# Kernel optimization log

Hardware: AMD Instinct MI355X
Metric: run time of the kernel (lower is better)

Reference implementation:

```python
import jax, jax.numpy as jnp
import numpy as np

N_NODES = 1000000


def setup_inputs() -> dict:
    key = jax.random.key(0)
    k1, k2, k3 = jax.random.split(key, 3)
    x = jax.random.normal(k1, (N_NODES, 16), dtype=jnp.float32)
    edge_index = jax.random.randint(k2, (2, 4000000), 0, N_NODES, dtype=jnp.int64)
    W = jax.random.normal(k3, (16, 16), dtype=jnp.float32) * (1.0 / np.sqrt(16.0))
    b = jnp.zeros((16,), dtype=jnp.float32)
    return {"x": x, "edge_index": edge_index, "W": W, "b": b}


def reference(x, edge_index, W, b):
    # GCNConv forward: out = D^{-1/2} (A + I) D^{-1/2} (x @ W) + b
    n = x.shape[0]
    row, col = edge_index[0], edge_index[1]  # src, dst

    h = x @ W  # [N, out]

    # degree on target nodes, including self-loops
    deg = jax.ops.segment_sum(jnp.ones_like(col, dtype=h.dtype), col, num_segments=n) + 1.0
    dinv = jax.lax.rsqrt(deg)  # deg >= 1 thanks to self-loops

    # per-edge symmetric normalization, gather-scale-scatter
    norm = dinv[row] * dinv[col]  # [E]
    msgs = h[row] * norm[:, None]  # [E, out]
    agg = jax.ops.segment_sum(msgs, col, num_segments=n)

    # self-loop contribution: norm_ii = dinv[i]^2
    out = agg + h * (dinv * dinv)[:, None] + b
    return out
```

## Files before the change

### kernel.cpp

```cpp
#include <hip/hip_runtime.h>


#define F 16
#define TILE 2048
#define TSHIFT 11
#define NBMAX 512
#define CAP 9728
#define EPT 19
#define CHUNK 8192
#define CUR_STRIDE 16

static __device__ __forceinline__ unsigned short f2bf(float f) {
    unsigned u = __float_as_uint(f);
    unsigned r = (u + 0x7FFFu + ((u >> 16) & 1u)) >> 16;
    return (unsigned short)r;
}
static __device__ __forceinline__ float bf2f(unsigned short u) {
    return __uint_as_float(((unsigned)u) << 16);
}

static __device__ __forceinline__ int excl_scan_512(int s, int t, int* wsum) {
    int lane = t & 63, wv = t >> 6;
    int incl = s;
    #pragma unroll
    for (int off = 1; off < 64; off <<= 1) {
        int y = __shfl_up(incl, off, 64);
        if (lane >= off) incl += y;
    }
    if (lane == 63) wsum[wv] = incl;
    __syncthreads();
    int woff = 0;
    #pragma unroll
    for (int w = 0; w < 8; w++) {
        int v = wsum[w];
        if (w < wv) woff += v;
    }
    return woff + incl - s;
}

__global__ void init_kernel(int* __restrict__ cursor, int nbuck) {
    int b = blockIdx.x * blockDim.x + threadIdx.x;
    if (b < nbuck) cursor[b * CUR_STRIDE] = b * CAP;
}

__global__ void __launch_bounds__(512)
bin_kernel(const int* __restrict__ row, const int* __restrict__ col,
           int* __restrict__ cursor, unsigned* __restrict__ adj, int E, int nbuck) {
    __shared__ int hist[NBMAX];
    __shared__ int lstart[NBMAX];
    __shared__ int slotBase[NBMAX];
    __shared__ int wsum[8];
    __shared__ unsigned sortedE[CHUNK];

    int t = threadIdx.x;
    hist[t] = 0;
    __syncthreads();

    int base = blockIdx.x * CHUNK;
    int nE = E - base; if (nE > CHUNK) nE = CHUNK;

    int c[16], r[16];
    #pragma unroll
    for (int q = 0; q < 16; q++) {
        int i = t + q * 512;
        if (i < nE) {
            c[q] = col[base + i];
            r[q] = row[base + i];
        } else { c[q] = -1; r[q] = 0; }
    }
    #pragma unroll
    for (int q = 0; q < 16; q++)
        if (c[q] >= 0) atomicAdd(&hist[c[q] >> TSHIFT], 1);
    __syncthreads();

    int s = hist[t];
    int excl = excl_scan_512(s, t, wsum);
    lstart[t] = excl;
    hist[t]   = excl;
    if (s > 0 && t < nbuck)
        slotBase[t] = atomicAdd(&cursor[t * CUR_STRIDE], s);
    __syncthreads();

    #pragma unroll
    for (int q = 0; q < 16; q++) {
        if (c[q] >= 0) {
            int bk = c[q] >> TSHIFT;
            int li = atomicAdd(&hist[bk], 1);
            sortedE[li] = (((unsigned)(c[q] & (TILE - 1))) << 20) | (unsigned)r[q];
        }
    }
    __syncthreads();

    for (int i = t; i < nE; i += 512) {
        int lo = 0, hi = NBMAX;
        #pragma unroll
        for (int it = 0; it < 9; it++) {
            int mid = (lo + hi) >> 1;
            if (lstart[mid] <= i) lo = mid; else hi = mid;
        }
        int bk = lo;
        int g = slotBase[bk] + (i - lstart[bk]);
        if (g < (bk + 1) * CAP) adj[g] = sortedE[i];
    }
}

__global__ void __launch_bounds__(512)
csr_node_kernel(const int* __restrict__ cursor, unsigned* __restrict__ adj,
                const float* __restrict__ x, const float* __restrict__ W,
                int2* __restrict__ pd, unsigned short* __restrict__ hs, int N) {
    __shared__ unsigned srt[CAP];
    __shared__ int hist[TILE];
    __shared__ int lstart[TILE];
    __shared__ int cnt2[TILE];
    __shared__ int wsum[8];
    __shared__ float sW[256];

    int t = threadIdx.x, b = blockIdx.x;
    if (t < 256) sW[t] = W[t];
    for (int i = t; i < TILE; i += 512) { hist[i] = 0; cnt2[i] = 0; }
    __syncthreads();

    int base = b * CAP;
    int cnt_total = cursor[b * CUR_STRIDE] - base;
    if (cnt_total > CAP) cnt_total = CAP;

    unsigned e[EPT];
    #pragma unroll
    for (int q = 0; q < EPT; q++) {
        int i = t + q * 512;
        if (i < cnt_total) {
            unsigned ee = adj[base + i];
            e[q] = ee;
            atomicAdd(&hist[ee >> 20], 1);
        } else e[q] = 0xFFFFFFFFu;
    }
    __syncthreads();

    int a0 = hist[4 * t], a1 = hist[4 * t + 1];
    int a2 = hist[4 * t + 2], a3 = hist[4 * t + 3];
    int s = a0 + a1 + a2 + a3;
    int excl = excl_scan_512(s, t, wsum);
    lstart[4 * t]     = excl;
    lstart[4 * t + 1] = excl + a0;
    lstart[4 * t + 2] = excl + a0 + a1;
    lstart[4 * t + 3] = excl + a0 + a1 + a2;
    __syncthreads();

    #pragma unroll
    for (int q = 0; q < EPT; q++) {
        if (e[q] != 0xFFFFFFFFu) {
            int cl = (int)(e[q] >> 20);
            int pos = lstart[cl] + atomicAdd(&cnt2[cl], 1);
            srt[pos] = e[q] & 0xFFFFFu;
        }
    }
    __syncthreads();
    #pragma unroll
    for (int q = 0; q < EPT; q++) {
        int i = t + q * 512;
        if (i < cnt_total) adj[base + i] = srt[i];
    }

    #pragma unroll
    for (int p = 0; p < 4; p++) {
        int local = p * 512 + t;
        int node = b * TILE + local;
        if (node >= N) continue;
        int dg = hist[local];
        pd[node] = make_int2(base + lstart[local], dg);
        float di = rsqrtf((float)dg + 1.0f);

        const float4* xr = (const float4*)(x + (size_t)node * F);
        float4 x0 = xr[0], x1 = xr[1], x2 = xr[2], x3 = xr[3];
        float xv[16] = {x0.x, x0.y, x0.z, x0.w, x1.x, x1.y, x1.z, x1.w,
                        x2.x, x2.y, x2.z, x2.w, x3.x, x3.y, x3.z, x3.w};
        float hv[16];
        #pragma unroll
        for (int j = 0; j < 16; j++) hv[j] = 0.f;
        #pragma unroll
        for (int k = 0; k < 16; k++) {
            float xk = xv[k];
            const float4* wr = (const float4*)(sW + k * 16);
            float4 w0 = wr[0], w1 = wr[1], w2 = wr[2], w3 = wr[3];
            hv[0]  += xk * w0.x; hv[1]  += xk * w0.y; hv[2]  += xk * w0.z; hv[3]  += xk * w0.w;
            hv[4]  += xk * w1.x; hv[5]  += xk * w1.y; hv[6]  += xk * w1.z; hv[7]  += xk * w1.w;
            hv[8]  += xk * w2.x; hv[9]  += xk * w2.y; hv[10] += xk * w2.z; hv[11] += xk * w2.w;
            hv[12] += xk * w3.x; hv[13] += xk * w3.y; hv[14] += xk * w3.z; hv[15] += xk * w3.w;
        }
        unsigned pkk[8];
        #pragma unroll
        for (int q = 0; q < 8; q++)
            pkk[q] = (unsigned)f2bf(hv[2*q] * di) | ((unsigned)f2bf(hv[2*q+1] * di) << 16);
        uint4* hp = (uint4*)(hs + (size_t)node * F);
        hp[0] = make_uint4(pkk[0], pkk[1], pkk[2], pkk[3]);
        hp[1] = make_uint4(pkk[4], pkk[5], pkk[6], pkk[7]);
    }
}

__global__ void __launch_bounds__(256)
gather_kernel(const int2* __restrict__ pd, const unsigned* __restrict__ adj,
              const unsigned short* __restrict__ hs, const float* __restrict__ bias,
              float* __restrict__ out, int N) {
    int tid = blockIdx.x * blockDim.x + threadIdx.x;
    int g = tid >> 4;
    int j = tid & 15;
    if (g >= N) return;

    int2 p = pd[g];
    int p0 = p.x, d = p.y;
    int end = p0 + d;

    float a0 = bf2f(hs[(size_t)g * F + j]);
    float a1 = 0.f;
    int k = p0;
    for (; k + 1 < end; k += 2) {
        unsigned r0 = adj[k];
        unsigned r1 = adj[k + 1];
        a0 += bf2f(hs[(size_t)r0 * F + j]);
        a1 += bf2f(hs[(size_t)r1 * F + j]);
    }
    if (k < end) a1 += bf2f(hs[(size_t)adj[k] * F + j]);

    float di = rsqrtf((float)d + 1.0f);
    out[(size_t)g * F + j] = di * (a0 + a1) + bias[j];
}

extern "C" void kernel_launch(void* const* d_in, const int* in_sizes, int n_in,
                              void* d_out, int out_size, void* d_ws, size_t ws_size,
                              hipStream_t stream) {
    const float* x  = (const float*)d_in[0];
    const int*   ei = (const int*)d_in[1];
    const float* W  = (const float*)d_in[2];
    const float* b  = (const float*)d_in[3];

    int N = in_sizes[0] / F;
    int E = in_sizes[1] / 2;
    const int* row = ei;
    const int* col = ei + E;

    float* out = (float*)d_out;
    int nbuck = (N + TILE - 1) / TILE;

    auto align_up = [](size_t v) { return (v + 255) & ~(size_t)255; };
    char* ws = (char*)d_ws;
    size_t off = 0;
    int* cursor = (int*)(ws + off);          off = align_up(off + (size_t)nbuck * CUR_STRIDE * 4);
    unsigned* adj = (unsigned*)(ws + off);   off = align_up(off + (size_t)nbuck * CAP * 4);
    int2* pd = (int2*)(ws + off);            off = align_up(off + (size_t)N * 8);
    unsigned short* hs = (unsigned short*)(ws + off); off = align_up(off + (size_t)N * F * 2);

    init_kernel<<<(nbuck + 255) / 256, 256, 0, stream>>>(cursor, nbuck);
    bin_kernel <<<(E + CHUNK - 1) / CHUNK, 512, 0, stream>>>(row, col, cursor, adj, E, nbuck);
    csr_node_kernel<<<nbuck, 512, 0, stream>>>(cursor, adj, x, W, pd, hs, N);

    long long gthreads = (long long)N * F;
    gather_kernel<<<(int)((gthreads + 255) / 256), 256, 0, stream>>>
        (pd, adj, hs, b, out, N);
}
```

Measured before the change: 298.8 us.

## Fuse per-bucket CSR sort into gather, compute degrees via global atomics

```diff
diff --git a/kernel.cpp b/kernel.cpp
--- a/kernel.cpp
+++ b/kernel.cpp
@@ -6,9 +6,10 @@
 #define TSHIFT 11
 #define NBMAX 512
 #define CAP 9728
-#define EPT 19
 #define CHUNK 8192
 #define CUR_STRIDE 16
+#define GT 1024
+#define GEPT 10
 
 static __device__ __forceinline__ unsigned short f2bf(float f) {
     unsigned u = __float_as_uint(f);
@@ -38,14 +39,36 @@
     return woff + incl - s;
 }
 
-__global__ void init_kernel(int* __restrict__ cursor, int nbuck) {
-    int b = blockIdx.x * blockDim.x + threadIdx.x;
-    if (b < nbuck) cursor[b * CUR_STRIDE] = b * CAP;
+static __device__ __forceinline__ int excl_scan_1024(int s, int t, int* wsum) {
+    int lane = t & 63, wv = t >> 6;
+    int incl = s;
+    #pragma unroll
+    for (int off = 1; off < 64; off <<= 1) {
+        int y = __shfl_up(incl, off, 64);
+        if (lane >= off) incl += y;
+    }
+    if (lane == 63) wsum[wv] = incl;
+    __syncthreads();
+    int woff = 0;
+    #pragma unroll
+    for (int w = 0; w < 16; w++) {
+        int v = wsum[w];
+        if (w < wv) woff += v;
+    }
+    return woff + incl - s;
+}
+
+__global__ void init_kernel(int* __restrict__ cursor, int nbuck,
+                            int* __restrict__ deg, int N) {
+    int i = blockIdx.x * blockDim.x + threadIdx.x;
+    if (i < nbuck) cursor[i * CUR_STRIDE] = i * CAP;
+    if (i < N) deg[i] = 0;
 }
 
 __global__ void __launch_bounds__(512)
 bin_kernel(const int* __restrict__ row, const int* __restrict__ col,
-           int* __restrict__ cursor, unsigned* __restrict__ adj, int E, int nbuck) {
+           int* __restrict__ cursor, unsigned* __restrict__ adj,
+           int* __restrict__ deg, int E, int nbuck) {
     __shared__ int hist[NBMAX];
     __shared__ int lstart[NBMAX];
     __shared__ int slotBase[NBMAX];
@@ -69,8 +92,12 @@
         } else { c[q] = -1; r[q] = 0; }
     }
     #pragma unroll
-    for (int q = 0; q < 16; q++)
-        if (c[q] >= 0) atomicAdd(&hist[c[q] >> TSHIFT], 1);
+    for (int q = 0; q < 16; q++) {
+        if (c[q] >= 0) {
+            atomicAdd(&hist[c[q] >> TSHIFT], 1);
+            atomicAdd(&deg[c[q]], 1);
+        }
+    }
     __syncthreads();
 
     int s = hist[t];
@@ -104,125 +131,119 @@
     }
 }
 
-__global__ void __launch_bounds__(512)
-csr_node_kernel(const int* __restrict__ cursor, unsigned* __restrict__ adj,
-                const float* __restrict__ x, const float* __restrict__ W,
-                int2* __restrict__ pd, unsigned short* __restrict__ hs, int N) {
+__global__ void __launch_bounds__(256)
+transform_kernel(const int* __restrict__ deg, const float* __restrict__ x,
+                 const float* __restrict__ W, unsigned short* __restrict__ hs,
+                 int N) {
+    __shared__ float sW[256];
+    int t = threadIdx.x;
+    sW[t] = W[t];
+    __syncthreads();
+
+    int node = blockIdx.x * 256 + t;
+    if (node >= N) return;
+
+    float di = rsqrtf((float)deg[node] + 1.0f);
+
+    const float4* xr = (const float4*)(x + (size_t)node * F);
+    float4 x0 = xr[0], x1 = xr[1], x2 = xr[2], x3 = xr[3];
+    float xv[16] = {x0.x, x0.y, x0.z, x0.w, x1.x, x1.y, x1.z, x1.w,
+                    x2.x, x2.y, x2.z, x2.w, x3.x, x3.y, x3.z, x3.w};
+    float hv[16];
+    #pragma unroll
+    for (int j = 0; j < 16; j++) hv[j] = 0.f;
+    #pragma unroll
+    for (int k = 0; k < 16; k++) {
+        float xk = xv[k];
+        const float4* wr = (const float4*)(sW + k * 16);
+        float4 w0 = wr[0], w1 = wr[1], w2 = wr[2], w3 = wr[3];
+        hv[0]  += xk * w0.x; hv[1]  += xk * w0.y; hv[2]  += xk * w0.z; hv[3]  += xk * w0.w;
+        hv[4]  += xk * w1.x; hv[5]  += xk * w1.y; hv[6]  += xk * w1.z; hv[7]  += xk * w1.w;
+        hv[8]  += xk * w2.x; hv[9]  += xk * w2.y; hv[10] += xk * w2.z; hv[11] += xk * w2.w;
+        hv[12] += xk * w3.x; hv[13] += xk * w3.y; hv[14] += xk * w3.z; hv[15] += xk * w3.w;
+    }
+    unsigned pkk[8];
+    #pragma unroll
+    for (int q = 0; q < 8; q++)
+        pkk[q] = (unsigned)f2bf(hv[2*q] * di) | ((unsigned)f2bf(hv[2*q+1] * di) << 16);
+    uint4* hp = (uint4*)(hs + (size_t)node * F);
+    hp[0] = make_uint4(pkk[0], pkk[1], pkk[2], pkk[3]);
+    hp[1] = make_uint4(pkk[4], pkk[5], pkk[6], pkk[7]);
+}
+
+__global__ void __launch_bounds__(GT, 8)
+fused_gather_kernel(const int* __restrict__ cursor, const unsigned* __restrict__ adj,
+                    const unsigned short* __restrict__ hs,
+                    const float* __restrict__ bias,
+                    float* __restrict__ out, int N) {
     __shared__ unsigned srt[CAP];
+    __shared__ unsigned short rankbuf[CAP];
     __shared__ int hist[TILE];
-    __shared__ int lstart[TILE];
-    __shared__ int cnt2[TILE];
-    __shared__ int wsum[8];
-    __shared__ float sW[256];
+    __shared__ int wsum[16];
 
     int t = threadIdx.x, b = blockIdx.x;
-    if (t < 256) sW[t] = W[t];
-    for (int i = t; i < TILE; i += 512) { hist[i] = 0; cnt2[i] = 0; }
+    #pragma unroll
+    for (int i = t; i < TILE; i += GT) hist[i] = 0;
     __syncthreads();
 
     int base = b * CAP;
     int cnt_total = cursor[b * CUR_STRIDE] - base;
     if (cnt_total > CAP) cnt_total = CAP;
 
-    unsigned e[EPT];
-    #pragma unroll
-    for (int q = 0; q < EPT; q++) {
-        int i = t + q * 512;
+    unsigned e[GEPT];
+    #pragma unroll
+    for (int q = 0; q < GEPT; q++) {
+        int i = t + q * GT;
         if (i < cnt_total) {
             unsigned ee = adj[base + i];
             e[q] = ee;
-            atomicAdd(&hist[ee >> 20], 1);
+            rankbuf[i] = (unsigned short)atomicAdd(&hist[ee >> 20], 1);
         } else e[q] = 0xFFFFFFFFu;
     }
     __syncthreads();
 
-    int a0 = hist[4 * t], a1 = hist[4 * t + 1];
-    int a2 = hist[4 * t + 2], a3 = hist[4 * t + 3];
-    int s = a0 + a1 + a2 + a3;
-    int excl = excl_scan_512(s, t, wsum);
-    lstart[4 * t]     = excl;
-    lstart[4 * t + 1] = excl + a0;
-    lstart[4 * t + 2] = excl + a0 + a1;
-    lstart[4 * t + 3] = excl + a0 + a1 + a2;
-    __syncthreads();
-
-    #pragma unroll
-    for (int q = 0; q < EPT; q++) {
+    int a0 = hist[2 * t], a1 = hist[2 * t + 1];
+    int s = a0 + a1;
+    int excl = excl_scan_1024(s, t, wsum);
+    hist[2 * t]     = excl;
+    hist[2 * t + 1] = excl + a0;
+    __syncthreads();
+
+    #pragma unroll
+    for (int q = 0; q < GEPT; q++) {
         if (e[q] != 0xFFFFFFFFu) {
+            int i = t + q * GT;
             int cl = (int)(e[q] >> 20);
-            int pos = lstart[cl] + atomicAdd(&cnt2[cl], 1);
+            int pos = hist[cl] + (int)rankbuf[i];
             srt[pos] = e[q] & 0xFFFFFu;
         }
     }
     __syncthreads();
-    #pragma unroll
-    for (int q = 0; q < EPT; q++) {
-        int i = t + q * 512;
-        if (i < cnt_total) adj[base + i] = srt[i];
-    }
-
-    #pragma unroll
-    for (int p = 0; p < 4; p++) {
-        int local = p * 512 + t;
-        int node = b * TILE + local;
+
+    int j = t & 15;
+    int slot = t >> 4;
+    for (int it = 0; it < TILE / (GT / 16); it++) {
+        int n = slot + it * (GT / 16);
+        int node = b * TILE + n;
         if (node >= N) continue;
-        int dg = hist[local];
-        pd[node] = make_int2(base + lstart[local], dg);
-        float di = rsqrtf((float)dg + 1.0f);
-
-        const float4* xr = (const float4*)(x + (size_t)node * F);
-        float4 x0 = xr[0], x1 = xr[1], x2 = xr[2], x3 = xr[3];
-        float xv[16] = {x0.x, x0.y, x0.z, x0.w, x1.x, x1.y, x1.z, x1.w,
-                        x2.x, x2.y, x2.z, x2.w, x3.x, x3.y, x3.z, x3.w};
-        float hv[16];
-        #pragma unroll
-        for (int j = 0; j < 16; j++) hv[j] = 0.f;
-        #pragma unroll
-        for (int k = 0; k < 16; k++) {
-            float xk = xv[k];
-            const float4* wr = (const float4*)(sW + k * 16);
-            float4 w0 = wr[0], w1 = wr[1], w2 = wr[2], w3 = wr[3];
-            hv[0]  += xk * w0.x; hv[1]  += xk * w0.y; hv[2]  += xk * w0.z; hv[3]  += xk * w0.w;
-            hv[4]  += xk * w1.x; hv[5]  += xk * w1.y; hv[6]  += xk * w1.z; hv[7]  += xk * w1.w;
-            hv[8]  += xk * w2.x; hv[9]  += xk * w2.y; hv[10] += xk * w2.z; hv[11] += xk * w2.w;
-            hv[12] += xk * w3.x; hv[13] += xk * w3.y; hv[14] += xk * w3.z; hv[15] += xk * w3.w;
-        }
-        unsigned pkk[8];
-        #pragma unroll
-        for (int q = 0; q < 8; q++)
-            pkk[q] = (unsigned)f2bf(hv[2*q] * di) | ((unsigned)f2bf(hv[2*q+1] * di) << 16);
-        uint4* hp = (uint4*)(hs + (size_t)node * F);
-        hp[0] = make_uint4(pkk[0], pkk[1], pkk[2], pkk[3]);
-        hp[1] = make_uint4(pkk[4], pkk[5], pkk[6], pkk[7]);
-    }
-}
-
-__global__ void __launch_bounds__(256)
-gather_kernel(const int2* __restrict__ pd, const unsigned* __restrict__ adj,
-              const unsigned short* __restrict__ hs, const float* __restrict__ bias,
-              float* __restrict__ out, int N) {
-    int tid = blockIdx.x * blockDim.x + threadIdx.x;
-    int g = tid >> 4;
-    int j = tid & 15;
-    if (g >= N) return;
-
-    int2 p = pd[g];
-    int p0 = p.x, d = p.y;
-    int end = p0 + d;
-
-    float a0 = bf2f(hs[(size_t)g * F + j]);
-    float a1 = 0.f;
-    int k = p0;
-    for (; k + 1 < end; k += 2) {
-        unsigned r0 = adj[k];
-        unsigned r1 = adj[k + 1];
-        a0 += bf2f(hs[(size_t)r0 * F + j]);
-        a1 += bf2f(hs[(size_t)r1 * F + j]);
-    }
-    if (k < end) a1 += bf2f(hs[(size_t)adj[k] * F + j]);
-
-    float di = rsqrtf((float)d + 1.0f);
-    out[(size_t)g * F + j] = di * (a0 + a1) + bias[j];
+        int p0 = hist[n];
+        int p1 = (n == TILE - 1) ? cnt_total : hist[n + 1];
+        int d = p1 - p0;
+
+        float a0 = bf2f(hs[(size_t)node * F + j]);
+        float a1 = 0.f;
+        int k = p0;
+        for (; k + 1 < p1; k += 2) {
+            unsigned r0 = srt[k];
+            unsigned r1 = srt[k + 1];
+            a0 += bf2f(hs[(size_t)r0 * F + j]);
+            a1 += bf2f(hs[(size_t)r1 * F + j]);
+        }
+        if (k < p1) a1 += bf2f(hs[(size_t)srt[k] * F + j]);
+
+        float di = rsqrtf((float)d + 1.0f);
+        out[(size_t)node * F + j] = di * (a0 + a1) + bias[j];
+    }
 }
 
 extern "C" void kernel_launch(void* const* d_in, const int* in_sizes, int n_in,
@@ -246,14 +267,11 @@
     size_t off = 0;
     int* cursor = (int*)(ws + off);          off = align_up(off + (size_t)nbuck * CUR_STRIDE * 4);
     unsigned* adj = (unsigned*)(ws + off);   off = align_up(off + (size_t)nbuck * CAP * 4);
-    int2* pd = (int2*)(ws + off);            off = align_up(off + (size_t)N * 8);
+    int* deg = (int*)(ws + off);             off = align_up(off + (size_t)N * 4);
     unsigned short* hs = (unsigned short*)(ws + off); off = align_up(off + (size_t)N * F * 2);
 
-    init_kernel<<<(nbuck + 255) / 256, 256, 0, stream>>>(cursor, nbuck);
-    bin_kernel <<<(E + CHUNK - 1) / CHUNK, 512, 0, stream>>>(row, col, cursor, adj, E, nbuck);
-    csr_node_kernel<<<nbuck, 512, 0, stream>>>(cursor, adj, x, W, pd, hs, N);
-
-    long long gthreads = (long long)N * F;
-    gather_kernel<<<(int)((gthreads + 255) / 256), 256, 0, stream>>>
-        (pd, adj, hs, b, out, N);
-}
+    init_kernel<<<(N + 255) / 256, 256, 0, stream>>>(cursor, nbuck, deg, N);
+    bin_kernel <<<(E + CHUNK - 1) / CHUNK, 512, 0, stream>>>(row, col, cursor, adj, deg, E, nbuck);
+    transform_kernel<<<(N + 255) / 256, 256, 0, stream>>>(deg, x, W, hs, N);
+    fused_gather_kernel<<<nbuck, GT, 0, stream>>>(cursor, adj, hs, b, out, N);
+}
```

Result: slower. 402.6 us (+34.7%).

## Move per-bucket CSR sort into gather kernel using shared-memory adjacency

Applied to the files above, without the earlier changes.

```diff
diff --git a/kernel.cpp b/kernel.cpp
--- a/kernel.cpp
+++ b/kernel.cpp
@@ -6,9 +6,9 @@
 #define TSHIFT 11
 #define NBMAX 512
 #define CAP 9728
-#define EPT 19
 #define CHUNK 8192
 #define CUR_STRIDE 16
+#define GT 1024
 
 static __device__ __forceinline__ unsigned short f2bf(float f) {
     unsigned u = __float_as_uint(f);
@@ -39,8 +39,8 @@
 }
 
 __global__ void init_kernel(int* __restrict__ cursor, int nbuck) {
-    int b = blockIdx.x * blockDim.x + threadIdx.x;
-    if (b < nbuck) cursor[b * CUR_STRIDE] = b * CAP;
+    int i = blockIdx.x * blockDim.x + threadIdx.x;
+    if (i < nbuck) cursor[i * CUR_STRIDE] = i * CAP;
 }
 
 __global__ void __launch_bounds__(512)
@@ -105,70 +105,41 @@
 }
 
 __global__ void __launch_bounds__(512)
-csr_node_kernel(const int* __restrict__ cursor, unsigned* __restrict__ adj,
+degxform_kernel(const int* __restrict__ cursor, const unsigned* __restrict__ adj,
                 const float* __restrict__ x, const float* __restrict__ W,
-                int2* __restrict__ pd, unsigned short* __restrict__ hs, int N) {
-    __shared__ unsigned srt[CAP];
+                unsigned short* __restrict__ lst_g, unsigned short* __restrict__ hs,
+                int N) {
     __shared__ int hist[TILE];
-    __shared__ int lstart[TILE];
-    __shared__ int cnt2[TILE];
     __shared__ int wsum[8];
     __shared__ float sW[256];
 
     int t = threadIdx.x, b = blockIdx.x;
     if (t < 256) sW[t] = W[t];
-    for (int i = t; i < TILE; i += 512) { hist[i] = 0; cnt2[i] = 0; }
+    for (int i = t; i < TILE; i += 512) hist[i] = 0;
     __syncthreads();
 
     int base = b * CAP;
     int cnt_total = cursor[b * CUR_STRIDE] - base;
     if (cnt_total > CAP) cnt_total = CAP;
 
-    unsigned e[EPT];
-    #pragma unroll
-    for (int q = 0; q < EPT; q++) {
-        int i = t + q * 512;
-        if (i < cnt_total) {
-            unsigned ee = adj[base + i];
-            e[q] = ee;
-            atomicAdd(&hist[ee >> 20], 1);
-        } else e[q] = 0xFFFFFFFFu;
-    }
+    for (int i = t; i < cnt_total; i += 512)
+        atomicAdd(&hist[adj[base + i] >> 20], 1);
     __syncthreads();
 
     int a0 = hist[4 * t], a1 = hist[4 * t + 1];
     int a2 = hist[4 * t + 2], a3 = hist[4 * t + 3];
     int s = a0 + a1 + a2 + a3;
     int excl = excl_scan_512(s, t, wsum);
-    lstart[4 * t]     = excl;
-    lstart[4 * t + 1] = excl + a0;
-    lstart[4 * t + 2] = excl + a0 + a1;
-    lstart[4 * t + 3] = excl + a0 + a1 + a2;
-    __syncthreads();
-
-    #pragma unroll
-    for (int q = 0; q < EPT; q++) {
-        if (e[q] != 0xFFFFFFFFu) {
-            int cl = (int)(e[q] >> 20);
-            int pos = lstart[cl] + atomicAdd(&cnt2[cl], 1);
-            srt[pos] = e[q] & 0xFFFFFu;
-        }
-    }
-    __syncthreads();
-    #pragma unroll
-    for (int q = 0; q < EPT; q++) {
-        int i = t + q * 512;
-        if (i < cnt_total) adj[base + i] = srt[i];
-    }
+    unsigned l0 = (unsigned)excl, l1 = l0 + a0, l2 = l1 + a1, l3 = l2 + a2;
+    *(uint2*)(lst_g + (size_t)b * TILE + 4 * t) =
+        make_uint2(l0 | (l1 << 16), l2 | (l3 << 16));
 
     #pragma unroll
     for (int p = 0; p < 4; p++) {
         int local = p * 512 + t;
         int node = b * TILE + local;
         if (node >= N) continue;
-        int dg = hist[local];
-        pd[node] = make_int2(base + lstart[local], dg);
-        float di = rsqrtf((float)dg + 1.0f);
+        float di = rsqrtf((float)hist[local] + 1.0f);
 
         const float4* xr = (const float4*)(x + (size_t)node * F);
         float4 x0 = xr[0], x1 = xr[1], x2 = xr[2], x3 = xr[3];
@@ -197,32 +168,60 @@
     }
 }
 
-__global__ void __launch_bounds__(256)
-gather_kernel(const int2* __restrict__ pd, const unsigned* __restrict__ adj,
-              const unsigned short* __restrict__ hs, const float* __restrict__ bias,
-              float* __restrict__ out, int N) {
-    int tid = blockIdx.x * blockDim.x + threadIdx.x;
-    int g = tid >> 4;
-    int j = tid & 15;
-    if (g >= N) return;
-
-    int2 p = pd[g];
-    int p0 = p.x, d = p.y;
-    int end = p0 + d;
-
-    float a0 = bf2f(hs[(size_t)g * F + j]);
-    float a1 = 0.f;
-    int k = p0;
-    for (; k + 1 < end; k += 2) {
-        unsigned r0 = adj[k];
-        unsigned r1 = adj[k + 1];
-        a0 += bf2f(hs[(size_t)r0 * F + j]);
-        a1 += bf2f(hs[(size_t)r1 * F + j]);
-    }
-    if (k < end) a1 += bf2f(hs[(size_t)adj[k] * F + j]);
-
-    float di = rsqrtf((float)d + 1.0f);
-    out[(size_t)g * F + j] = di * (a0 + a1) + bias[j];
+__global__ void __launch_bounds__(GT, 8)
+fused_gather_kernel(const int* __restrict__ cursor, const unsigned* __restrict__ adj,
+                    const unsigned short* __restrict__ lst_g,
+                    const unsigned short* __restrict__ hs,
+                    const float* __restrict__ bias,
+                    float* __restrict__ out, int N) {
+    __shared__ unsigned srt[CAP];
+    __shared__ unsigned short lst[TILE + 2];
+    __shared__ int cnt2[TILE / 2];
+
+    int t = threadIdx.x, b = blockIdx.x;
+    int base = b * CAP;
+    int cnt_total = cursor[b * CUR_STRIDE] - base;
+    if (cnt_total > CAP) cnt_total = CAP;
+
+    for (int i = t; i < TILE / 2; i += GT) cnt2[i] = 0;
+    for (int i = t; i < TILE; i += GT) lst[i] = lst_g[(size_t)b * TILE + i];
+    if (t == 0) lst[TILE] = (unsigned short)cnt_total;
+    __syncthreads();
+
+    for (int i = t; i < cnt_total; i += GT) {
+        unsigned e = adj[base + i];
+        int cl = (int)(e >> 20);
+        int sh = (cl & 1) * 16;
+        unsigned ret = atomicAdd((unsigned*)&cnt2[cl >> 1], 1u << sh);
+        int rank = (int)((ret >> sh) & 0xFFFFu);
+        srt[(int)lst[cl] + rank] = e & 0xFFFFFu;
+    }
+    __syncthreads();
+
+    int j = t & 15;
+    int slot = t >> 4;
+    for (int it = 0; it < TILE / (GT / 16); it++) {
+        int n = slot + it * (GT / 16);
+        int node = b * TILE + n;
+        if (node >= N) continue;
+        int p0 = lst[n];
+        int p1 = lst[n + 1];
+        int d = p1 - p0;
+
+        float a0 = bf2f(hs[(size_t)node * F + j]);
+        float a1 = 0.f;
+        int k = p0;
+        for (; k + 1 < p1; k += 2) {
+            unsigned r0 = srt[k];
+            unsigned r1 = srt[k + 1];
+            a0 += bf2f(hs[(size_t)r0 * F + j]);
+            a1 += bf2f(hs[(size_t)r1 * F + j]);
+        }
+        if (k < p1) a1 += bf2f(hs[(size_t)srt[k] * F + j]);
+
+        float di = rsqrtf((float)d + 1.0f);
+        out[(size_t)node * F + j] = di * (a0 + a1) + bias[j];
+    }
 }
 
 extern "C" void kernel_launch(void* const* d_in, const int* in_sizes, int n_in,
@@ -246,14 +245,11 @@
     size_t off = 0;
     int* cursor = (int*)(ws + off);          off = align_up(off + (size_t)nbuck * CUR_STRIDE * 4);
     unsigned* adj = (unsigned*)(ws + off);   off = align_up(off + (size_t)nbuck * CAP * 4);
-    int2* pd = (int2*)(ws + off);            off = align_up(off + (size_t)N * 8);
-    unsigned short* hs = (unsigned short*)(ws + off); off = align_up(off + (size_t)N * F * 2);
+    unsigned short* lst_g = (unsigned short*)(ws + off); off = align_up(off + (size_t)nbuck * TILE * 2);
+    unsigned short* hs = (unsigned short*)(ws + off);    off = align_up(off + (size_t)N * F * 2);
 
     init_kernel<<<(nbuck + 255) / 256, 256, 0, stream>>>(cursor, nbuck);
     bin_kernel <<<(E + CHUNK - 1) / CHUNK, 512, 0, stream>>>(row, col, cursor, adj, E, nbuck);
-    csr_node_kernel<<<nbuck, 512, 0, stream>>>(cursor, adj, x, W, pd, hs, N);
-
-    long long gthreads = (long long)N * F;
-    gather_kernel<<<(int)((gthreads + 255) / 256), 256, 0, stream>>>
-        (pd, adj, hs, b, out, N);
-}
+    degxform_kernel<<<nbuck, 512, 0, stream>>>(cursor, adj, x, W, lst_g, hs, N);
+    fused_gather_kernel<<<nbuck, GT, 0, stream>>>(cursor, adj, lst_g, hs, b, out, N);
+}
```

After: 260.1 us. 1.15x faster.
